# Kernel tuning notes

Hardware: AMD Instinct MI355X
Metric: run time of the kernel (lower is better)

Reference implementation:

```python
import jax, jax.numpy as jnp
import numpy as np

B, H, W, D = 64, 32, 32, 64
K = 1024  # codebook_size


def setup_inputs() -> dict:
    key = jax.random.key(0)
    kz, ke = jax.random.split(key)
    z = jax.random.normal(kz, (B, H, W, D), dtype=jnp.float32)
    embeddings = 0.02 * jax.random.normal(ke, (K, D), dtype=jnp.float32)
    return {"z": z, "embeddings": embeddings}


def reference(z, embeddings):
    # Flatten spatial/batch dims: (N, D) with N = B*H*W
    z_flat = z.reshape(-1, z.shape[-1])
    # Squared euclidean distances via ||a||^2 + ||b||^2 - 2 a.b  -> (N, K)
    distances = (jnp.sum(z_flat ** 2, axis=1, keepdims=True)
                 + jnp.sum(embeddings ** 2, axis=1)
                 - 2.0 * jnp.dot(z_flat, embeddings.T))
    indices = jnp.argmin(distances, axis=1)  # (N,)
    quantized = embeddings[indices].reshape(z.shape)  # (B, H, W, D)
    indices = indices.reshape(z.shape[0], z.shape[1], z.shape[2])  # (B, H, W)
    return quantized, indices
```

## Files before the change

kernel.cpp:

```cpp
#include <hip/hip_runtime.h>

#define NPTS   65536
#define DDIM   64
#define KCODES 1024
#define QOUT_ELEMS (NPTS * DDIM)

typedef _Float16 half8    __attribute__((ext_vector_type(8)));
typedef float    floatx16 __attribute__((ext_vector_type(16)));
typedef unsigned int uint;

#define WS_EHP   0
#define WS_ELP   (128*1024)
#define WS_E2    (256*1024)

union H8U { half8 v; uint u[4]; };

__global__ void eprep_kernel(const float* __restrict__ emb, char* __restrict__ ws) {
    const int tid = threadIdx.x;
    const int w = tid >> 6, d = tid & 63;
    const int k = blockIdx.x * 4 + w;
    float v = emb[(size_t)k * DDIM + d];
    _Float16 h = (_Float16)v;
    _Float16 l = (_Float16)(v - (float)h);
    size_t off = (size_t)(k >> 5) * 4096 + (size_t)(d >> 3) * 512
               + (size_t)(k & 31) * 16 + (size_t)(d & 7) * 2;
    *(_Float16*)(ws + WS_EHP + off) = h;
    *(_Float16*)(ws + WS_ELP + off) = l;
    float s = v * v;
    #pragma unroll
    for (int m = 1; m < 64; m <<= 1) s += __shfl_xor(s, m, 64);
    if (d == 0) {
        _Float16 e2h = (_Float16)s;
        _Float16 e2l = (_Float16)(s - (float)e2h);
        unsigned short hb = *(unsigned short*)&e2h;
        unsigned short lb = *(unsigned short*)&e2l;
        ((uint*)(ws + WS_E2))[k] = (uint)hb | ((uint)lb << 16);
    }
}

#define MFMA(A,B,C) __builtin_amdgcn_mfma_f32_32x32x16_f16(A,B,C,0,0,0)

__global__ __launch_bounds__(256, 2) void vq_kernel(
    const float* __restrict__ z,
    const char* __restrict__ ws_c,
    const float* __restrict__ emb,
    float* __restrict__ out)
{
    const int tid  = threadIdx.x;
    const int lane = tid & 63;
    const int w    = __builtin_amdgcn_readfirstlane(tid >> 6);
    const int col  = lane & 31;
    const int sel8 = lane >> 5;
    const int pgrp = blockIdx.x;

    __shared__ int s_final[128];

    const int pt = pgrp * 128 + w * 32 + col;
    half8 ah[4], al[4];
    {
        const float* zrow = z + (size_t)pt * DDIM + sel8 * 8;
        #pragma unroll
        for (int ks = 0; ks < 4; ++ks) {
            float4 u0 = *(const float4*)(zrow + ks * 16);
            float4 u1 = *(const float4*)(zrow + ks * 16 + 4);
            float tv[8] = {u0.x, u0.y, u0.z, u0.w, u1.x, u1.y, u1.z, u1.w};
            #pragma unroll
            for (int j = 0; j < 8; ++j) {
                float a = -2.0f * tv[j];
                _Float16 hh = (_Float16)a;
                ah[ks][j] = hh;
                al[ks][j] = (_Float16)(a - (float)hh);
            }
        }
    }
    half8 ahE;
    { H8U t0; t0.u[0] = (sel8 == 0) ? 0x3C003C00u : 0u;
      t0.u[1] = t0.u[2] = t0.u[3] = 0u; ahE = t0.v; }

    const floatx16 zeroC = {};

    float best[16];
    int   bt[16];
    #pragma unroll
    for (int r = 0; r < 16; ++r) { best[r] = 3.4e38f; bt[r] = 0; }

    const int myoff = sel8 * 512 + col * 16;
    const char* ebase = ws_c + myoff;
    const uint* e2p   = (const uint*)(ws_c + WS_E2);

    half8 bhA[4], blA[4], bhB[4], blB[4];
    uint  eA, eB;

#define LOADT(T, BH, BL, E2) do {                                        \
    const char* _b = ebase + (size_t)(T) * 4096;                         \
    _Pragma("unroll")                                                    \
    for (int ks = 0; ks < 4; ++ks) {                                     \
        BH[ks] = *(const half8*)(_b + ks * 1024);                        \
        BL[ks] = *(const half8*)(_b + WS_ELP + ks * 1024);               \
    }                                                                    \
    E2 = e2p[(T) * 32 + col];                                            \
} while (0)

#define TILE(T, BH, BL, E2) do {                                         \
    H8U _u; _u.u[0] = (E2); _u.u[1] = _u.u[2] = _u.u[3] = 0u;            \
    __builtin_amdgcn_s_setprio(1);                                       \
    floatx16 _a0 = MFMA(ah[0], BH[0], zeroC);                            \
    _a0 = MFMA(ah[1], BH[1], _a0);                                       \
    _a0 = MFMA(ah[2], BH[2], _a0);                                       \
    _a0 = MFMA(ah[3], BH[3], _a0);                                       \
    _a0 = MFMA(ahE,   _u.v,  _a0);                                       \
    floatx16 _a1 = MFMA(ah[0], BL[0], zeroC);                            \
    _a1 = MFMA(ah[1], BL[1], _a1);                                       \
    _a1 = MFMA(ah[2], BL[2], _a1);                                       \
    _a1 = MFMA(ah[3], BL[3], _a1);                                       \
    _a1 = MFMA(al[0], BH[0], _a1);                                       \
    _a1 = MFMA(al[1], BH[1], _a1);                                       \
    _a1 = MFMA(al[2], BH[2], _a1);                                       \
    _a1 = MFMA(al[3], BH[3], _a1);                                       \
    __builtin_amdgcn_s_setprio(0);                                       \
    _Pragma("unroll")                                                    \
    for (int r = 0; r < 16; ++r) {                                       \
        float _d = _a0[r] + _a1[r];                                      \
        bool  _c = _d < best[r];       \
        best[r] = _c ? _d  : best[r];                                    \
        bt[r]   = _c ? (T) : bt[r];                                      \
    }                                                                    \
} while (0)

    LOADT(0, bhA, blA, eA);
    for (int t = 0; t < 32; t += 2) {
        LOADT(t + 1, bhB, blB, eB);
        TILE(t, bhA, blA, eA);
        int tn = (t + 2 < 32) ? (t + 2) : 0;
        LOADT(tn, bhA, blA, eA);
        TILE(t + 1, bhB, blB, eB);
    }

#undef LOADT
#undef TILE

    int code[16];
    #pragma unroll
    for (int r = 0; r < 16; ++r) code[r] = bt[r] * 32 + col;
    #pragma unroll
    for (int m = 1; m < 32; m <<= 1) {
        #pragma unroll
        for (int r = 0; r < 16; ++r) {
            float ov = __shfl_xor(best[r], m, 64);
            int   oc = __shfl_xor(code[r], m, 64);
            bool c = (ov < best[r]) || (ov == best[r] && oc < code[r]);
            best[r] = c ? ov : best[r];
            code[r] = c ? oc : code[r];
        }
    }
    if (col == 0) {
        #pragma unroll
        for (int r = 0; r < 16; ++r) {
            int row = (r & 3) + 8 * (r >> 2) + 4 * sel8;
            s_final[w * 32 + row] = code[r];
        }
    }
    __syncthreads();

    if (tid < 128)
        out[QOUT_ELEMS + (size_t)pgrp * 128 + tid] = (float)s_final[tid];
    float4* outq = (float4*)out;
    const float4* emb4 = (const float4*)emb;
    #pragma unroll
    for (int it = 0; it < 8; ++it) {
        int f  = it * 256 + tid;
        int p  = f >> 4;
        int d4 = f & 15;
        int ks = s_final[p];
        outq[((size_t)pgrp * 128 + p) * (DDIM / 4) + d4] =
            emb4[(size_t)ks * (DDIM / 4) + d4];
    }
}

extern "C" void kernel_launch(void* const* d_in, const int* in_sizes, int n_in,
                              void* d_out, int out_size, void* d_ws, size_t ws_size,
                              hipStream_t stream) {
    const float* z   = (const float*)d_in[0];
    const float* emb = (const float*)d_in[1];
    float* out = (float*)d_out;
    char* ws = (char*)d_ws;

    eprep_kernel<<<KCODES / 4, 256, 0, stream>>>(emb, ws);
    vq_kernel<<<NPTS / 128, 256, 0, stream>>>(z, ws, emb, out);
}
```

Before: 108.1 us.

## Drop e2 MFMA, add codebook norm in FP32, interleave two accumulator chains

The codebook squared norm is now stored as plain fp32 and added in the VALU argmin update, replacing the extra MFMA that folded a split-fp16 norm into the accumulator. The two MFMA chains are interleaved so independent accumulators can issue back to back, and the error terms are split across both chains. The loop is kept rolled with scheduling barriers between half-iterations to control instruction ordering. This cuts one MFMA per tile and shortens dependency chains, but adds 16 VALU adds per tile and may limit compiler scheduling freedom.

```diff
diff --git a/kernel.cpp b/kernel.cpp
--- a/kernel.cpp
+++ b/kernel.cpp
@@ -13,8 +13,6 @@
 #define WS_ELP   (128*1024)
 #define WS_E2    (256*1024)
 
-union H8U { half8 v; uint u[4]; };
-
 __global__ void eprep_kernel(const float* __restrict__ emb, char* __restrict__ ws) {
     const int tid = threadIdx.x;
     const int w = tid >> 6, d = tid & 63;
@@ -29,13 +27,7 @@
     float s = v * v;
     #pragma unroll
     for (int m = 1; m < 64; m <<= 1) s += __shfl_xor(s, m, 64);
-    if (d == 0) {
-        _Float16 e2h = (_Float16)s;
-        _Float16 e2l = (_Float16)(s - (float)e2h);
-        unsigned short hb = *(unsigned short*)&e2h;
-        unsigned short lb = *(unsigned short*)&e2l;
-        ((uint*)(ws + WS_E2))[k] = (uint)hb | ((uint)lb << 16);
-    }
+    if (d == 0) ((float*)(ws + WS_E2))[k] = s;
 }
 
 #define MFMA(A,B,C) __builtin_amdgcn_mfma_f32_32x32x16_f16(A,B,C,0,0,0)
@@ -73,9 +65,6 @@
             }
         }
     }
-    half8 ahE;
-    { H8U t0; t0.u[0] = (sel8 == 0) ? 0x3C003C00u : 0u;
-      t0.u[1] = t0.u[2] = t0.u[3] = 0u; ahE = t0.v; }
 
     const floatx16 zeroC = {};
 
@@ -85,57 +74,55 @@
     for (int r = 0; r < 16; ++r) { best[r] = 3.4e38f; bt[r] = 0; }
 
     const int myoff = sel8 * 512 + col * 16;
-    const char* ebase = ws_c + myoff;
-    const uint* e2p   = (const uint*)(ws_c + WS_E2);
+    const char*  ebase = ws_c + myoff;
+    const float* e2p   = (const float*)(ws_c + WS_E2);
 
-    half8 bhA[4], blA[4], bhB[4], blB[4];
-    uint  eA, eB;
-
-#define LOADT(T, BH, BL, E2) do {                                        \
+#define LOADT(BH, BL, E2, T) do {                                        \
     const char* _b = ebase + (size_t)(T) * 4096;                         \
-    _Pragma("unroll")                                                    \
-    for (int ks = 0; ks < 4; ++ks) {                                     \
-        BH[ks] = *(const half8*)(_b + ks * 1024);                        \
-        BL[ks] = *(const half8*)(_b + WS_ELP + ks * 1024);               \
-    }                                                                    \
+    BH[0] = *(const half8*)(_b);                                         \
+    BH[1] = *(const half8*)(_b + 1024);                                  \
+    BH[2] = *(const half8*)(_b + 2048);                                  \
+    BH[3] = *(const half8*)(_b + 3072);                                  \
+    BL[0] = *(const half8*)(_b + WS_ELP);                                \
+    BL[1] = *(const half8*)(_b + WS_ELP + 1024);                         \
+    BL[2] = *(const half8*)(_b + WS_ELP + 2048);                         \
+    BL[3] = *(const half8*)(_b + WS_ELP + 3072);                         \
     E2 = e2p[(T) * 32 + col];                                            \
 } while (0)
 
 #define TILE(T, BH, BL, E2) do {                                         \
-    H8U _u; _u.u[0] = (E2); _u.u[1] = _u.u[2] = _u.u[3] = 0u;            \
     __builtin_amdgcn_s_setprio(1);                                       \
-    floatx16 _a0 = MFMA(ah[0], BH[0], zeroC);                            \
-    _a0 = MFMA(ah[1], BH[1], _a0);                                       \
-    _a0 = MFMA(ah[2], BH[2], _a0);                                       \
-    _a0 = MFMA(ah[3], BH[3], _a0);                                       \
-    _a0 = MFMA(ahE,   _u.v,  _a0);                                       \
-    floatx16 _a1 = MFMA(ah[0], BL[0], zeroC);                            \
-    _a1 = MFMA(ah[1], BL[1], _a1);                                       \
-    _a1 = MFMA(ah[2], BL[2], _a1);                                       \
-    _a1 = MFMA(ah[3], BL[3], _a1);                                       \
-    _a1 = MFMA(al[0], BH[0], _a1);                                       \
-    _a1 = MFMA(al[1], BH[1], _a1);                                       \
-    _a1 = MFMA(al[2], BH[2], _a1);                                       \
-    _a1 = MFMA(al[3], BH[3], _a1);                                       \
+    floatx16 c0 = MFMA(ah[0], BH[0], zeroC);                             \
+    floatx16 c1 = MFMA(ah[0], BL[0], zeroC);                             \
+    c0 = MFMA(ah[1], BH[1], c0);  c1 = MFMA(ah[1], BL[1], c1);           \
+    c0 = MFMA(ah[2], BH[2], c0);  c1 = MFMA(ah[2], BL[2], c1);           \
+    c0 = MFMA(ah[3], BH[3], c0);  c1 = MFMA(ah[3], BL[3], c1);           \
+    c0 = MFMA(al[0], BH[0], c0);  c1 = MFMA(al[2], BH[2], c1);           \
+    c0 = MFMA(al[1], BH[1], c0);  c1 = MFMA(al[3], BH[3], c1);           \
     __builtin_amdgcn_s_setprio(0);                                       \
     _Pragma("unroll")                                                    \
     for (int r = 0; r < 16; ++r) {                                       \
-        float _d = _a0[r] + _a1[r];                                      \
-        bool  _c = _d < best[r];       \
-        best[r] = _c ? _d  : best[r];                                    \
-        bt[r]   = _c ? (T) : bt[r];                                      \
+        float d = (c0[r] + c1[r]) + (E2);                                \
+        bool c = d < best[r];           \
+        best[r] = c ? d   : best[r];                                     \
+        bt[r]   = c ? (T) : bt[r];                                       \
     }                                                                    \
 } while (0)
 
-    LOADT(0, bhA, blA, eA);
+    half8 bhA[4], blA[4], bhB[4], blB[4];
+    float e2A, e2B;
+
+    LOADT(bhA, blA, e2A, 0);
+    #pragma unroll 1
     for (int t = 0; t < 32; t += 2) {
-        LOADT(t + 1, bhB, blB, eB);
-        TILE(t, bhA, blA, eA);
-        int tn = (t + 2 < 32) ? (t + 2) : 0;
-        LOADT(tn, bhA, blA, eA);
-        TILE(t + 1, bhB, blB, eB);
+        LOADT(bhB, blB, e2B, t + 1);
+        TILE(t, bhA, blA, e2A);
+        __builtin_amdgcn_sched_barrier(0);
+
+        LOADT(bhA, blA, e2A, (t + 2) & 31);
+        TILE(t + 1, bhB, blB, e2B);
+        __builtin_amdgcn_sched_barrier(0);
     }
-
 #undef LOADT
 #undef TILE
 
```

After: 104.1 us. -3.8%, faster.
